# Kernel optimization log

Measured on AMD Instinct MI355X. Metric: run time of the kernel, lower is better.

Reference implementation:

```python
import jax, jax.numpy as jnp
import numpy as np

RES = (64, 64, 64)      # sim.res
INV_DX = 64.0           # sim.inv_dx (n_grid = 64)
P_MASS = 1.0            # sim.p_mass
N = 4_000_000           # n_particles


def setup_inputs() -> dict:
    key = jax.random.key(0)
    k1, k2 = jax.random.split(key)
    # positions in [0.05, 0.95)^3 so the 3x3x3 B-spline stencil stays in-grid
    x = jax.random.uniform(k1, (N, 3), jnp.float32) * 0.9 + 0.05
    x_ref = jax.random.uniform(k2, (N, 3), jnp.float32) * 0.9 + 0.05
    return {"x": x, "x_ref": x_ref}


def _density(x):
    # x: [N, 3] particle positions in [0, 1)
    xs = x * INV_DX
    base = jnp.floor(xs - 0.5).astype(jnp.int32)  # [N, 3]; positions > 0 so floor == trunc (.int() in torch)
    fx = xs - base.astype(x.dtype)                # [N, 3]
    # quadratic B-spline weights, stacked -> [3, N, 3]
    w = jnp.stack([0.5 * (1.5 - fx) ** 2,
                   0.75 - (fx - 1.0) ** 2,
                   0.5 * (fx - 0.5) ** 2])
    density = jnp.zeros(RES, x.dtype)
    # scatter-add over the 27 stencil offsets (equivalent to the unique/mask dedup sum)
    for i in range(3):
        for j in range(3):
            for k in range(3):
                weight = w[i, :, 0] * w[j, :, 1] * w[k, :, 2]  # [N]
                idx = base + jnp.array([i, j, k], jnp.int32)   # [N, 3]
                density = density.at[idx[:, 0], idx[:, 1], idx[:, 2]].add(weight * P_MASS)
    return density


def reference(x, x_ref):
    density = _density(x)
    density_ref = _density(x_ref)
    return jnp.abs(density - density_ref).sum()
```

## Files before the change

kernel.cpp:

```cpp
#include <hip/hip_runtime.h>

#define NRES 64
#define GRID_CELLS (NRES * NRES * NRES)
#define TILE_CELLS 16384
#define TPB 1024
#define NBLK 512
#define ZBINS 64
#define NSLABS2 32
#define GC 8
#define CAP 150016u
#define MAXC 32
#define FXS 4194304.0f
#define INV_FXS (1.0f / 4194304.0f)
#define QS 2097152.0f
typedef unsigned long long u64;
typedef unsigned u32;
typedef unsigned short u16;


__device__ __forceinline__ u32 quantc(float v) {
    return (u32)(v * QS + 0.5f);
}
__device__ __forceinline__ int cell_from_q(u32 q) {
    float s = (float)q * (1.0f / 32768.0f);
    int c = (int)(s - 0.5f);
    return min(max(c, 0), 63);
}

__global__ void init_cursors_kernel(u32* __restrict__ cursor) {
    if (threadIdx.x < ZBINS) cursor[threadIdx.x] = (u32)threadIdx.x * CAP;
}

__global__ __launch_bounds__(TPB)
void fused_fill_kernel(const float* __restrict__ x, const float* __restrict__ xr,
                       int n, u32* __restrict__ cursor, u64* __restrict__ bins) {
    __shared__ u32 h[ZBINS];
    __shared__ u32 cur[ZBINS];
    if (threadIdx.x < ZBINS) h[threadIdx.x] = 0;
    __syncthreads();

    const int Q = n >> 2;
    const int GQ = 2 * Q;
    const int per = (GQ + NBLK - 1) / NBLK;
    const int g0 = blockIdx.x * per;
    const int g1 = min(GQ, g0 + per);

    for (int g = g0 + (int)threadIdx.x; g < g1; g += TPB) {
        const float* __restrict__ p = (g < Q) ? (x + 12 * (size_t)g)
                                              : (xr + 12 * (size_t)(g - Q));
        float z0 = p[2], z1 = p[5], z2 = p[8], z3 = p[11];
        atomicAdd(&h[cell_from_q(quantc(z0))], 1u);
        atomicAdd(&h[cell_from_q(quantc(z1))], 1u);
        atomicAdd(&h[cell_from_q(quantc(z2))], 1u);
        atomicAdd(&h[cell_from_q(quantc(z3))], 1u);
    }
    __syncthreads();
    if (threadIdx.x < ZBINS) {
        u32 c = h[threadIdx.x];
        cur[threadIdx.x] = c ? atomicAdd(&cursor[threadIdx.x], c)
                             : (u32)threadIdx.x * CAP;
    }
    __syncthreads();

    for (int g = g0 + (int)threadIdx.x; g < g1; g += TPB) {
        int inx = (g < Q);
        const float* __restrict__ p = inx ? (x + 12 * (size_t)g)
                                          : (xr + 12 * (size_t)(g - Q));
        float4 a = ((const float4*)p)[0];
        float4 b = ((const float4*)p)[1];
        float4 c = ((const float4*)p)[2];
        u64 sgn = inx ? 0ull : (1ull << 63);
        float px[4] = {a.x, a.w, b.z, c.y};
        float py[4] = {a.y, b.x, b.w, c.z};
        float pz[4] = {a.z, b.y, c.x, c.w};
#pragma unroll
        for (int q = 0; q < 4; ++q) {
            u32 xq = quantc(px[q]);
            u32 yq = quantc(py[q]);
            u32 zq = quantc(pz[q]);
            u64 ent = (u64)xq | ((u64)yq << 21) | ((u64)zq << 42) | sgn;
            int bz = cell_from_q(zq);
            u32 slot = atomicAdd(&cur[bz], 1u);
            if (slot < (u32)(bz + 1) * CAP) bins[slot] = ent;
        }
    }
}

__global__ __launch_bounds__(TPB)
void bin_scatter_kernel(const u64* __restrict__ bins,
                        const u32* __restrict__ cursor,
                        int* __restrict__ partial) {
    __shared__ int tile[TILE_CELLS];
    const int slab  = blockIdx.x / GC;
    const int chunk = blockIdx.x - slab * GC;

    for (int i = threadIdx.x; i < TILE_CELLS / 4; i += TPB)
        reinterpret_cast<int4*>(tile)[i] = make_int4(0, 0, 0, 0);
    __syncthreads();

    const u32 b0 = (u32)(2 * slab), b1 = b0 + 1;
    u32 c0 = cursor[b0] - b0 * CAP; if (c0 > CAP) c0 = CAP;
    u32 c1 = cursor[b1] - b1 * CAP; if (c1 > CAP) c1 = CAP;
    u32 cnt = c0 + c1;
    u32 per = (cnt + (u32)GC - 1u) / (u32)GC;
    u32 i0 = (u32)chunk * per;
    u32 i1 = i0 + per;
    if (i1 > cnt) i1 = cnt;

    for (u32 i = i0 + threadIdx.x; i < i1; i += TPB) {
        u32 idx = (i < c0) ? (b0 * CAP + i) : (b1 * CAP + (i - c0));
        u64 v = bins[idx];
        float xs = (float)(u32)(v & 0x1FFFFFu) * (1.0f / 32768.0f);
        float ys = (float)(u32)((v >> 21) & 0x1FFFFFu) * (1.0f / 32768.0f);
        float zs = (float)(u32)((v >> 42) & 0x1FFFFFu) * (1.0f / 32768.0f);
        float fsgn = (v >> 63) ? -FXS : FXS;

        int bx = (int)(xs - 0.5f);
        int by = (int)(ys - 0.5f);
        int bz = (int)(zs - 0.5f);
        float fx = xs - (float)bx, fy = ys - (float)by, fz = zs - (float)bz;

        float wx0 = 0.5f * (1.5f - fx) * (1.5f - fx);
        float wx1 = 0.75f - (fx - 1.0f) * (fx - 1.0f);
        float wx2 = 0.5f * (fx - 0.5f) * (fx - 0.5f);
        float wy0 = 0.5f * (1.5f - fy) * (1.5f - fy);
        float wy1 = 0.75f - (fy - 1.0f) * (fy - 1.0f);
        float wy2 = 0.5f * (fy - 0.5f) * (fy - 0.5f);
        float wzv[3];
        wzv[0] = 0.5f * (1.5f - fz) * (1.5f - fz);
        wzv[1] = 0.75f - (fz - 1.0f) * (fz - 1.0f);
        wzv[2] = 0.5f * (fz - 0.5f) * (fz - 0.5f);

        float wxy[9];
        wxy[0] = wx0 * wy0; wxy[1] = wx0 * wy1; wxy[2] = wx0 * wy2;
        wxy[3] = wx1 * wy0; wxy[4] = wx1 * wy1; wxy[5] = wx1 * wy2;
        wxy[6] = wx2 * wy0; wxy[7] = wx2 * wy1; wxy[8] = wx2 * wy2;

        int basexy = bx * 64 + by;
        int zlo = bz - 2 * slab;
#pragma unroll
        for (int k = 0; k < 3; ++k) {
            float wzS = wzv[k] * fsgn;
            int a = (zlo + k) * 4096 + basexy;
#pragma unroll
            for (int i2 = 0; i2 < 3; ++i2)
#pragma unroll
                for (int j2 = 0; j2 < 3; ++j2)
                    atomicAdd(&tile[a + i2 * 64 + j2],
                              __float2int_rn(wxy[i2 * 3 + j2] * wzS));
        }
    }
    __syncthreads();

    int* __restrict__ dst = partial + (size_t)blockIdx.x * TILE_CELLS;
    for (int i = threadIdx.x; i < TILE_CELLS / 4; i += TPB)
        reinterpret_cast<int4*>(dst)[i] = reinterpret_cast<const int4*>(tile)[i];
}

__global__ void int_reduce_kernel(const int* __restrict__ partial,
                                  float* __restrict__ out) {
    int tid = blockIdx.x * blockDim.x + threadIdx.x;
    int z  = tid >> 12;
    int xy = tid & 4095;
    int s0 = z >> 1, zl0 = z & 1;
    int sum = 0;
    const int* __restrict__ p0 =
        partial + (size_t)(s0 * GC) * TILE_CELLS + zl0 * 4096 + xy;
#pragma unroll
    for (int g = 0; g < GC; ++g) sum += p0[(size_t)g * TILE_CELLS];
    if (s0 > 0) {
        const int* __restrict__ p1 =
            partial + (size_t)((s0 - 1) * GC) * TILE_CELLS + (zl0 + 2) * 4096 + xy;
#pragma unroll
        for (int g = 0; g < GC; ++g) sum += p1[(size_t)g * TILE_CELLS];
    }
    float v = fabsf((float)sum) * INV_FXS;
#pragma unroll
    for (int off = 32; off > 0; off >>= 1) v += __shfl_down(v, off, 64);
    __shared__ float wsum[4];
    int lane = threadIdx.x & 63, wid = threadIdx.x >> 6;
    if (lane == 0) wsum[wid] = v;
    __syncthreads();
    if (threadIdx.x == 0) atomicAdd(out, wsum[0] + wsum[1] + wsum[2] + wsum[3]);
}


__global__ __launch_bounds__(TPB)
void slab_scatter_kernel(const float* __restrict__ x,
                         const float* __restrict__ xr,
                         int n, int C, float* __restrict__ partial) {
    __shared__ float tile[TILE_CELLS];
    const int slab  = blockIdx.x / C;
    const int chunk = blockIdx.x - slab * C;
    const int z0 = slab * 4;

    for (int i = threadIdx.x; i < TILE_CELLS; i += TPB) tile[i] = 0.0f;
    __syncthreads();

    const int per = (n + C - 1) / C;
    const int p0 = chunk * per;
    const int p1 = min(n, p0 + per);

    for (int f = 0; f < 2; ++f) {
        const float* __restrict__ p = f ? xr : x;
        const float sgn = f ? -1.0f : 1.0f;
        for (int i = p0 + (int)threadIdx.x; i < p1; i += TPB) {
            float zs = p[3 * i + 2] * 64.0f;
            int bz = (int)floorf(zs - 0.5f);
            int zlo = bz - z0;
            if (zlo > 3 || zlo + 2 < 0) continue;

            float xs = p[3 * i + 0] * 64.0f;
            float ys = p[3 * i + 1] * 64.0f;
            int bx = (int)floorf(xs - 0.5f);
            int by = (int)floorf(ys - 0.5f);
            float fx = xs - (float)bx, fy = ys - (float)by, fz = zs - (float)bz;

            float wx0 = 0.5f * (1.5f - fx) * (1.5f - fx);
            float wx1 = 0.75f - (fx - 1.0f) * (fx - 1.0f);
            float wx2 = 0.5f * (fx - 0.5f) * (fx - 0.5f);
            float wy0 = 0.5f * (1.5f - fy) * (1.5f - fy);
            float wy1 = 0.75f - (fy - 1.0f) * (fy - 1.0f);
            float wy2 = 0.5f * (fy - 0.5f) * (fy - 0.5f);
            float wzv[3];
            wzv[0] = 0.5f * (1.5f - fz) * (1.5f - fz);
            wzv[1] = 0.75f - (fz - 1.0f) * (fz - 1.0f);
            wzv[2] = 0.5f * (fz - 0.5f) * (fz - 0.5f);

            float wxy[9];
            wxy[0] = sgn * wx0 * wy0; wxy[1] = sgn * wx0 * wy1; wxy[2] = sgn * wx0 * wy2;
            wxy[3] = sgn * wx1 * wy0; wxy[4] = sgn * wx1 * wy1; wxy[5] = sgn * wx1 * wy2;
            wxy[6] = sgn * wx2 * wy0; wxy[7] = sgn * wx2 * wy1; wxy[8] = sgn * wx2 * wy2;

            int base = (bx * 64 + by) * 4;
#pragma unroll
            for (int k = 0; k < 3; ++k) {
                int zl = zlo + k;
                if (zl < 0 || zl >= 4) continue;
                float wzk = wzv[k];
                int a = base + zl;
#pragma unroll
                for (int i2 = 0; i2 < 3; ++i2)
#pragma unroll
                    for (int j2 = 0; j2 < 3; ++j2)
                        atomicAdd(&tile[a + i2 * 256 + j2 * 4], wxy[i2 * 3 + j2] * wzk);
            }
        }
    }
    __syncthreads();

    float* __restrict__ dst = partial + (size_t)chunk * GRID_CELLS;
    for (int t = threadIdx.x; t < NRES * NRES; t += TPB) {
        float4 v = *reinterpret_cast<const float4*>(&tile[t * 4]);
        *reinterpret_cast<float4*>(&dst[t * 64 + z0]) = v;
    }
}

__global__ void reduce_kernel(const float* __restrict__ partial, int C,
                              float* __restrict__ out) {
    int cell = blockIdx.x * blockDim.x + threadIdx.x;
    float s = 0.0f;
    for (int c = 0; c < C; ++c) s += partial[(size_t)c * GRID_CELLS + cell];
    s = fabsf(s);
#pragma unroll
    for (int off = 32; off > 0; off >>= 1) s += __shfl_down(s, off, 64);
    __shared__ float wsum[4];
    int lane = threadIdx.x & 63, wid = threadIdx.x >> 6;
    if (lane == 0) wsum[wid] = s;
    __syncthreads();
    if (threadIdx.x == 0) atomicAdd(out, wsum[0] + wsum[1] + wsum[2] + wsum[3]);
}

extern "C" void kernel_launch(void* const* d_in, const int* in_sizes, int n_in,
                              void* d_out, int out_size, void* d_ws, size_t ws_size,
                              hipStream_t stream) {
    const float* x  = (const float*)d_in[0];
    const float* xr = (const float*)d_in[1];
    float* out = (float*)d_out;
    char* ws = (char*)d_ws;

    int n = in_sizes[0] / 3;

    const size_t OFF_CUR  = 0;
    const size_t OFF_BINS = 4096;
    const size_t binsBytes = (size_t)ZBINS * CAP * sizeof(u64);
    const size_t OFF_PART = OFF_BINS + binsBytes;
    const size_t partBytes = (size_t)NSLABS2 * GC * TILE_CELLS * 4;
    const size_t gridBytes = (size_t)GRID_CELLS * sizeof(float);

    hipMemsetAsync(out, 0, sizeof(float), stream);

    if ((n & 3) == 0 && (u32)(2 * n) <= ZBINS * (CAP - 10000u)
        && ws_size >= OFF_PART + partBytes) {
        u32* cursor  = (u32*)(ws + OFF_CUR);
        u64* bins    = (u64*)(ws + OFF_BINS);
        int* partial = (int*)(ws + OFF_PART);

        init_cursors_kernel<<<1, 64, 0, stream>>>(cursor);
        fused_fill_kernel<<<NBLK, TPB, 0, stream>>>(x, xr, n, cursor, bins);
        bin_scatter_kernel<<<NSLABS2 * GC, TPB, 0, stream>>>(bins, cursor, partial);
        int_reduce_kernel<<<GRID_CELLS / 256, 256, 0, stream>>>(partial, out);
    } else {
        float* partial = (float*)ws;
        int C = (int)(ws_size / gridBytes);
        if (C > MAXC) C = MAXC;
        if (C < 1) C = 1;
        slab_scatter_kernel<<<16 * C, TPB, 0, stream>>>(x, xr, n, C, partial);
        reduce_kernel<<<GRID_CELLS / 256, 256, 0, stream>>>(partial, C, out);
    }
}
```

Measured before the change: 136.8 us.

## Stage binned particles in LDS and write coalesced per-bin runs in fill kernel

```diff
diff --git a/kernel.cpp b/kernel.cpp
--- a/kernel.cpp
+++ b/kernel.cpp
@@ -4,7 +4,8 @@
 #define GRID_CELLS (NRES * NRES * NRES)
 #define TILE_CELLS 16384
 #define TPB 1024
-#define NBLK 512
+#define QI 2
+#define FILL_QUADS (TPB * QI)
 #define ZBINS 64
 #define NSLABS2 32
 #define GC 8
@@ -27,61 +28,88 @@
     return min(max(c, 0), 63);
 }
 
-__global__ void init_cursors_kernel(u32* __restrict__ cursor) {
-    if (threadIdx.x < ZBINS) cursor[threadIdx.x] = (u32)threadIdx.x * CAP;
-}
-
 __global__ __launch_bounds__(TPB)
 void fused_fill_kernel(const float* __restrict__ x, const float* __restrict__ xr,
                        int n, u32* __restrict__ cursor, u64* __restrict__ bins) {
+    __shared__ u64 stage[FILL_QUADS * 4];
     __shared__ u32 h[ZBINS];
-    __shared__ u32 cur[ZBINS];
-    if (threadIdx.x < ZBINS) h[threadIdx.x] = 0;
+    __shared__ u32 lb[ZBINS];
+    __shared__ u32 gb[ZBINS];
+    const int tid = threadIdx.x;
+    if (tid < ZBINS) h[tid] = 0;
     __syncthreads();
 
     const int Q = n >> 2;
     const int GQ = 2 * Q;
-    const int per = (GQ + NBLK - 1) / NBLK;
-    const int g0 = blockIdx.x * per;
-    const int g1 = min(GQ, g0 + per);
-
-    for (int g = g0 + (int)threadIdx.x; g < g1; g += TPB) {
-        const float* __restrict__ p = (g < Q) ? (x + 12 * (size_t)g)
+    const int g0 = blockIdx.x * FILL_QUADS + tid;
+
+    u64 ent[QI][4];
+    u32 lsl[QI][4];
+    bool val[QI];
+
+#pragma unroll
+    for (int it = 0; it < QI; ++it) {
+        int g = g0 + it * TPB;
+        val[it] = (g < GQ);
+        if (val[it]) {
+            int inx = (g < Q);
+            const float* __restrict__ p = inx ? (x + 12 * (size_t)g)
                                               : (xr + 12 * (size_t)(g - Q));
-        float z0 = p[2], z1 = p[5], z2 = p[8], z3 = p[11];
-        atomicAdd(&h[cell_from_q(quantc(z0))], 1u);
-        atomicAdd(&h[cell_from_q(quantc(z1))], 1u);
-        atomicAdd(&h[cell_from_q(quantc(z2))], 1u);
-        atomicAdd(&h[cell_from_q(quantc(z3))], 1u);
-    }
-    __syncthreads();
-    if (threadIdx.x < ZBINS) {
-        u32 c = h[threadIdx.x];
-        cur[threadIdx.x] = c ? atomicAdd(&cursor[threadIdx.x], c)
-                             : (u32)threadIdx.x * CAP;
-    }
-    __syncthreads();
-
-    for (int g = g0 + (int)threadIdx.x; g < g1; g += TPB) {
-        int inx = (g < Q);
-        const float* __restrict__ p = inx ? (x + 12 * (size_t)g)
-                                          : (xr + 12 * (size_t)(g - Q));
-        float4 a = ((const float4*)p)[0];
-        float4 b = ((const float4*)p)[1];
-        float4 c = ((const float4*)p)[2];
-        u64 sgn = inx ? 0ull : (1ull << 63);
-        float px[4] = {a.x, a.w, b.z, c.y};
-        float py[4] = {a.y, b.x, b.w, c.z};
-        float pz[4] = {a.z, b.y, c.x, c.w};
-#pragma unroll
-        for (int q = 0; q < 4; ++q) {
-            u32 xq = quantc(px[q]);
-            u32 yq = quantc(py[q]);
-            u32 zq = quantc(pz[q]);
-            u64 ent = (u64)xq | ((u64)yq << 21) | ((u64)zq << 42) | sgn;
-            int bz = cell_from_q(zq);
-            u32 slot = atomicAdd(&cur[bz], 1u);
-            if (slot < (u32)(bz + 1) * CAP) bins[slot] = ent;
+            float4 a = ((const float4*)p)[0];
+            float4 b = ((const float4*)p)[1];
+            float4 c = ((const float4*)p)[2];
+            u64 sgn = inx ? 0ull : (1ull << 63);
+            float px[4] = {a.x, a.w, b.z, c.y};
+            float py[4] = {a.y, b.x, b.w, c.z};
+            float pz[4] = {a.z, b.y, c.x, c.w};
+#pragma unroll
+            for (int q = 0; q < 4; ++q) {
+                u32 xq = quantc(px[q]);
+                u32 yq = quantc(py[q]);
+                u32 zq = quantc(pz[q]);
+                ent[it][q] = (u64)xq | ((u64)yq << 21) | ((u64)zq << 42) | sgn;
+                int bz = cell_from_q(zq);
+                lsl[it][q] = atomicAdd(&h[bz], 1u);
+            }
+        }
+    }
+    __syncthreads();
+
+    if (tid < 64) {
+        u32 c = h[tid];
+        u32 acc = c;
+#pragma unroll
+        for (int off = 1; off < 64; off <<= 1) {
+            u32 o = __shfl_up(acc, off, 64);
+            if (tid >= off) acc += o;
+        }
+        lb[tid] = acc - c;
+        gb[tid] = c ? atomicAdd(&cursor[tid], c) : 0u;
+    }
+    __syncthreads();
+
+#pragma unroll
+    for (int it = 0; it < QI; ++it) {
+        if (val[it]) {
+#pragma unroll
+            for (int q = 0; q < 4; ++q) {
+                u64 v = ent[it][q];
+                int bz = cell_from_q((u32)((v >> 42) & 0x1FFFFFu));
+                stage[lb[bz] + lsl[it][q]] = v;
+            }
+        }
+    }
+    __syncthreads();
+
+    const int wid = tid >> 6, lane = tid & 63;
+    for (int b = wid; b < ZBINS; b += TPB / 64) {
+        u32 cnt = h[b];
+        u32 l0 = lb[b];
+        u32 g  = gb[b];
+        u64* __restrict__ dst = bins + (size_t)b * CAP;
+        for (u32 i = lane; i < cnt; i += 64) {
+            u32 slot = g + i;
+            if (slot < CAP) dst[slot] = stage[l0 + i];
         }
     }
 }
@@ -99,8 +127,8 @@
     __syncthreads();
 
     const u32 b0 = (u32)(2 * slab), b1 = b0 + 1;
-    u32 c0 = cursor[b0] - b0 * CAP; if (c0 > CAP) c0 = CAP;
-    u32 c1 = cursor[b1] - b1 * CAP; if (c1 > CAP) c1 = CAP;
+    u32 c0 = cursor[b0]; if (c0 > CAP) c0 = CAP;
+    u32 c1 = cursor[b1]; if (c1 > CAP) c1 = CAP;
     u32 cnt = c0 + c1;
     u32 per = (cnt + (u32)GC - 1u) / (u32)GC;
     u32 i0 = (u32)chunk * per;
@@ -296,8 +324,11 @@
         u64* bins    = (u64*)(ws + OFF_BINS);
         int* partial = (int*)(ws + OFF_PART);
 
-        init_cursors_kernel<<<1, 64, 0, stream>>>(cursor);
-        fused_fill_kernel<<<NBLK, TPB, 0, stream>>>(x, xr, n, cursor, bins);
+        int GQ = (n >> 2) * 2;
+        int fillBlocks = (GQ + FILL_QUADS - 1) / FILL_QUADS;
+
+        hipMemsetAsync(cursor, 0, ZBINS * sizeof(u32), stream);
+        fused_fill_kernel<<<fillBlocks, TPB, 0, stream>>>(x, xr, n, cursor, bins);
         bin_scatter_kernel<<<NSLABS2 * GC, TPB, 0, stream>>>(bins, cursor, partial);
         int_reduce_kernel<<<GRID_CELLS / 256, 256, 0, stream>>>(partial, out);
     } else {
```

New measurement: 122.0 us, median of 2. -10.9%, faster.
